# Kernel tuning notes

Hardware: AMD Instinct MI355X
Metric: run time of the kernel (lower is better)

The kernel has to match this reference:

```python
import jax, jax.numpy as jnp
import numpy as np

BATCH = 65536
NUM_OBS = 64
LATENT = 64
HID = (512, 512, 256)


def _mlp(x, W1, b1, W2, b2, W3, b3, W4, b4):
    # torch Linear: y = x @ W.T + b, ELU activations between hidden layers
    h = jax.nn.elu(x @ W1.T + b1)
    h = jax.nn.elu(h @ W2.T + b2)
    h = jax.nn.elu(h @ W3.T + b3)
    return h @ W4.T + b4  # [B, LATENT]


def setup_inputs() -> dict:
    key = jax.random.key(0)
    ks = jax.random.split(key, 9)
    def w(k, shape, fan_in):
        return jax.random.normal(k, shape, dtype=jnp.float32) * (1.0 / np.sqrt(fan_in))
    return {
        "x": jax.random.normal(ks[0], (BATCH, NUM_OBS), dtype=jnp.float32),
        "W1": w(ks[1], (HID[0], NUM_OBS), NUM_OBS),
        "b1": jnp.zeros((HID[0],), jnp.float32),
        "W2": w(ks[2], (HID[1], HID[0]), HID[0]),
        "b2": jnp.zeros((HID[1],), jnp.float32),
        "W3": w(ks[3], (HID[2], HID[1]), HID[1]),
        "b3": jnp.zeros((HID[2],), jnp.float32),
        "W4": w(ks[4], (LATENT, HID[2]), HID[2]),
        "b4": jnp.zeros((LATENT,), jnp.float32),
    }


def reference(x, W1, b1, W2, b2, W3, b3, W4, b4):
    sign = -1.0  # minimize=False -> sign = -1
    z = _mlp(x, W1, b1, W2, b2, W3, b3, W4, b4)          # [B, L]
    A = jnp.einsum('bi,bj->bij', z, z)                    # outer product [B, L, L]
    x_off = x - jnp.zeros_like(x)                         # offset_NN is zeros (no offset_hidden_dims)
    value = sign * jnp.einsum('bi,bij,bj->b', x_off, A, x_off)  # x^T A x, squeezed
    return value
```

## Files before the change

### kernel.cpp

```cpp
#include <hip/hip_runtime.h>


#define DEVI __device__ __forceinline__

typedef __attribute__((ext_vector_type(4))) float f32x4;
typedef __attribute__((ext_vector_type(8))) short bf16x8;

#define PADW 520
#define ROWS 64

DEVI short f2bf(float f) {
  unsigned u = __float_as_uint(f);
  u = u + 0x7fffu + ((u >> 16) & 1u);
  return (short)(u >> 16);
}

__global__ void cvtw_all_kernel(const float* __restrict__ W1, const float* __restrict__ W2,
                                const float* __restrict__ W3, const float* __restrict__ W4,
                                short* __restrict__ dst) {
  int i = blockIdx.x * blockDim.x + threadIdx.x;
  if (i >= 110592) return;
  const float* src;
  int off;
  if (i < 8192)        { src = W1; off = 0; }
  else if (i < 73728)  { src = W2; off = 8192; }
  else if (i < 106496) { src = W3; off = 73728; }
  else                 { src = W4; off = 106496; }
  float4 v = reinterpret_cast<const float4*>(src)[i - off];
  short4 o;
  o.x = f2bf(v.x); o.y = f2bf(v.y); o.z = f2bf(v.z); o.w = f2bf(v.w);
  reinterpret_cast<short4*>(dst)[i] = o;
}

template<int K, int NCT, bool DO_ELU>
DEVI void mlp_layer(const short* __restrict__ Wb, const float* __restrict__ bias,
                    short (&hb)[ROWS][PADW], int wn, int lane) {
  const int lr = lane & 15, kg = lane >> 4;
  const int c0 = wn * (NCT * 16);
  f32x4 acc[4][NCT] = {};
  for (int ks = 0; ks < K / 32; ++ks) {
    const int kk = ks * 32 + kg * 8;
    bf16x8 a[4], b[NCT];
#pragma unroll
    for (int rt = 0; rt < 4; ++rt)
      a[rt] = *reinterpret_cast<const bf16x8*>(&hb[rt * 16 + lr][kk]);
#pragma unroll
    for (int ct = 0; ct < NCT; ++ct)
      b[ct] = *reinterpret_cast<const bf16x8*>(&Wb[(c0 + ct * 16 + lr) * K + kk]);
#pragma unroll
    for (int rt = 0; rt < 4; ++rt)
#pragma unroll
      for (int ct = 0; ct < NCT; ++ct)
        acc[rt][ct] = __builtin_amdgcn_mfma_f32_16x16x32_bf16(a[rt], b[ct], acc[rt][ct], 0, 0, 0);
  }
  __syncthreads();
#pragma unroll
  for (int ct = 0; ct < NCT; ++ct) {
    const int col = c0 + ct * 16 + lr;
    const float bv = bias[col];
#pragma unroll
    for (int rt = 0; rt < 4; ++rt) {
#pragma unroll
      for (int j = 0; j < 4; ++j) {
        float v = acc[rt][ct][j] + bv;
        if (DO_ELU) v = v > 0.f ? v : (__expf(v) - 1.f);
        hb[rt * 16 + kg * 4 + j][col] = f2bf(v);
      }
    }
  }
  __syncthreads();
}

DEVI void final_layer(const short* __restrict__ W4b, const float* __restrict__ b4,
                      const float* __restrict__ xg, float* __restrict__ out,
                      short (&hb)[ROWS][PADW], int wid, int lane, int R0) {
  const int lr = lane & 15, kg = lane >> 4;
  const int r0 = wid * 16;
  f32x4 acc[4] = {};
  for (int ks = 0; ks < 8; ++ks) {
    const int kk = ks * 32 + kg * 8;
    bf16x8 a = *reinterpret_cast<const bf16x8*>(&hb[r0 + lr][kk]);
#pragma unroll
    for (int ct = 0; ct < 4; ++ct) {
      bf16x8 b = *reinterpret_cast<const bf16x8*>(&W4b[(ct * 16 + lr) * 256 + kk]);
      acc[ct] = __builtin_amdgcn_mfma_f32_16x16x32_bf16(a, b, acc[ct], 0, 0, 0);
    }
  }
  float bv[4];
#pragma unroll
  for (int ct = 0; ct < 4; ++ct) bv[ct] = b4[ct * 16 + lr];
#pragma unroll
  for (int j = 0; j < 4; ++j) {
    const int gr = R0 + r0 + kg * 4 + j;
    float p = 0.f;
#pragma unroll
    for (int ct = 0; ct < 4; ++ct)
      p += (acc[ct][j] + bv[ct]) * xg[gr * 64 + ct * 16 + lr];
    p += __shfl_xor(p, 1);
    p += __shfl_xor(p, 2);
    p += __shfl_xor(p, 4);
    p += __shfl_xor(p, 8);
    if (lr == 0) out[gr] = -p * p;
  }
}

__global__ __launch_bounds__(512, 4)
void mlp_fused_kernel(const float* __restrict__ x,
                      const short* __restrict__ Wb,
                      const float* __restrict__ b1, const float* __restrict__ b2,
                      const float* __restrict__ b3, const float* __restrict__ b4,
                      float* __restrict__ out) {
  __shared__ __align__(16) short hb[ROWS][PADW];
  const int tid = threadIdx.x;
  const int lane = tid & 63, wid = tid >> 6;
  const int R0 = blockIdx.x * ROWS;

#pragma unroll
  for (int s = 0; s < 2; ++s) {
    const int f = tid + s * 512;
    const int r = f >> 4, c4 = f & 15;
    float4 v = reinterpret_cast<const float4*>(x)[R0 * 16 + f];
    short4 o;
    o.x = f2bf(v.x); o.y = f2bf(v.y); o.z = f2bf(v.z); o.w = f2bf(v.w);
    *reinterpret_cast<short4*>(&hb[r][c4 * 4]) = o;
  }
  __syncthreads();

  const short* W1b = Wb;
  const short* W2b = Wb + 32768;
  const short* W3b = Wb + 32768 + 262144;
  const short* W4b = Wb + 32768 + 262144 + 131072;

  mlp_layer<64, 4, true>(W1b, b1, hb, wid, lane);
  mlp_layer<512, 4, true>(W2b, b2, hb, wid, lane);
  mlp_layer<512, 2, true>(W3b, b3, hb, wid, lane);
  if (wid < 4)
    final_layer(W4b, b4, x, out, hb, wid, lane, R0);
}

extern "C" void kernel_launch(void* const* d_in, const int* in_sizes, int n_in,
                              void* d_out, int out_size, void* d_ws, size_t ws_size,
                              hipStream_t stream) {
  const float* x  = (const float*)d_in[0];
  const float* W1 = (const float*)d_in[1];
  const float* b1 = (const float*)d_in[2];
  const float* W2 = (const float*)d_in[3];
  const float* b2 = (const float*)d_in[4];
  const float* W3 = (const float*)d_in[5];
  const float* b3 = (const float*)d_in[6];
  const float* W4 = (const float*)d_in[7];
  const float* b4 = (const float*)d_in[8];
  float* out = (float*)d_out;
  short* wsb = (short*)d_ws;

  cvtw_all_kernel<<<432, 256, 0, stream>>>(W1, W2, W3, W4, wsb);
  mlp_fused_kernel<<<1024, 512, 0, stream>>>(x, wsb, b1, b2, b3, b4, out);
}
```

Before: 194.8 us.

## Double-buffer weight k-slices in LDS via async global_load_lds prefetch

Weight tiles for each 32-wide k-step are now copied asynchronously into two swizzled LDS buffers with global_load_lds, and the next slice is prefetched while the current one feeds MFMA. Prefetching crosses layer boundaries, so the first slice of the next layer loads during the last step of the current one. The intent is to hide global and L2 latency on the weight operand and avoid bank conflicts through an XOR swizzle. The cost is an extra 64KB of LDS per block, which lowers occupancy (launch bounds drop from 4 to 2), and a block-wide barrier on every k-step. Each wave still consumes only its own columns, so the staging adds no data reuse.

```diff
diff --git a/kernel.cpp b/kernel.cpp
--- a/kernel.cpp
+++ b/kernel.cpp
@@ -32,13 +32,38 @@
   reinterpret_cast<short4*>(dst)[i] = o;
 }
 
-template<int K, int NCT, bool DO_ELU>
-DEVI void mlp_layer(const short* __restrict__ Wb, const float* __restrict__ bias,
-                    short (&hb)[ROWS][PADW], int wn, int lane) {
-  const int lr = lane & 15, kg = lane >> 4;
-  const int c0 = wn * (NCT * 16);
+DEVI void gld16(const void* g, void* l) {
+  __builtin_amdgcn_global_load_lds((const __attribute__((address_space(1))) void*)g,
+                                   (__attribute__((address_space(3))) void*)l, 16, 0, 0);
+}
+
+template<int COLS, int K>
+DEVI void stage_w(const short* __restrict__ W, int ks, short* dst, int tid) {
+#pragma unroll
+  for (int i = 0; i < COLS / 128; ++i) {
+    const int G = i * 512 + tid;
+    const int c = G >> 2, gp = G & 3;
+    const int g = gp ^ ((c >> 1) & 3);
+    gld16(W + c * K + ks * 32 + g * 8, dst + G * 8);
+  }
+}
+
+template<int K, int NCT, int NEXT_COLS, int NEXT_K>
+DEVI void hidden_layer(const short* __restrict__ W, const short* __restrict__ Wn,
+                       const float* __restrict__ bias,
+                       short (&hb)[ROWS][PADW], short* wta, short* wtb, int& cur,
+                       int tid, int wid, int lr, int kg) {
+  const int c0 = wid * (NCT * 16);
+  const int swz = (kg ^ ((lr >> 1) & 3)) * 16;
+  constexpr int NKS = K / 32;
   f32x4 acc[4][NCT] = {};
-  for (int ks = 0; ks < K / 32; ++ks) {
+  for (int ks = 0; ks < NKS; ++ks) {
+    short* nxt = cur ? wta : wtb;
+    const short* src = cur ? wtb : wta;
+    if (ks + 1 < NKS)
+      stage_w<NCT * 128, K>(W, ks + 1, nxt, tid);
+    else if constexpr (NEXT_COLS > 0)
+      stage_w<NEXT_COLS, NEXT_K>(Wn, 0, nxt, tid);
     const int kk = ks * 32 + kg * 8;
     bf16x8 a[4], b[NCT];
 #pragma unroll
@@ -46,14 +71,16 @@
       a[rt] = *reinterpret_cast<const bf16x8*>(&hb[rt * 16 + lr][kk]);
 #pragma unroll
     for (int ct = 0; ct < NCT; ++ct)
-      b[ct] = *reinterpret_cast<const bf16x8*>(&Wb[(c0 + ct * 16 + lr) * K + kk]);
+      b[ct] = *reinterpret_cast<const bf16x8*>(
+          (const char*)src + (c0 + ct * 16 + lr) * 64 + swz);
 #pragma unroll
     for (int rt = 0; rt < 4; ++rt)
 #pragma unroll
       for (int ct = 0; ct < NCT; ++ct)
         acc[rt][ct] = __builtin_amdgcn_mfma_f32_16x16x32_bf16(a[rt], b[ct], acc[rt][ct], 0, 0, 0);
+    __syncthreads();
+    cur ^= 1;
   }
-  __syncthreads();
 #pragma unroll
   for (int ct = 0; ct < NCT; ++ct) {
     const int col = c0 + ct * 16 + lr;
@@ -63,7 +90,7 @@
 #pragma unroll
       for (int j = 0; j < 4; ++j) {
         float v = acc[rt][ct][j] + bv;
-        if (DO_ELU) v = v > 0.f ? v : (__expf(v) - 1.f);
+        v = v > 0.f ? v : (__expf(v) - 1.f);
         hb[rt * 16 + kg * 4 + j][col] = f2bf(v);
       }
     }
@@ -104,16 +131,23 @@
   }
 }
 
-__global__ __launch_bounds__(512, 4)
+__global__ __launch_bounds__(512, 2)
 void mlp_fused_kernel(const float* __restrict__ x,
                       const short* __restrict__ Wb,
                       const float* __restrict__ b1, const float* __restrict__ b2,
                       const float* __restrict__ b3, const float* __restrict__ b4,
                       float* __restrict__ out) {
   __shared__ __align__(16) short hb[ROWS][PADW];
+  __shared__ __align__(16) short wt[2][512 * 32];
   const int tid = threadIdx.x;
   const int lane = tid & 63, wid = tid >> 6;
+  const int lr = lane & 15, kg = lane >> 4;
   const int R0 = blockIdx.x * ROWS;
+
+  const short* W1b = Wb;
+  const short* W2b = Wb + 32768;
+  const short* W3b = Wb + 32768 + 262144;
+  const short* W4b = Wb + 32768 + 262144 + 131072;
 
 #pragma unroll
   for (int s = 0; s < 2; ++s) {
@@ -124,16 +158,13 @@
     o.x = f2bf(v.x); o.y = f2bf(v.y); o.z = f2bf(v.z); o.w = f2bf(v.w);
     *reinterpret_cast<short4*>(&hb[r][c4 * 4]) = o;
   }
+  stage_w<512, 64>(W1b, 0, wt[0], tid);
   __syncthreads();
 
-  const short* W1b = Wb;
-  const short* W2b = Wb + 32768;
-  const short* W3b = Wb + 32768 + 262144;
-  const short* W4b = Wb + 32768 + 262144 + 131072;
-
-  mlp_layer<64, 4, true>(W1b, b1, hb, wid, lane);
-  mlp_layer<512, 4, true>(W2b, b2, hb, wid, lane);
-  mlp_layer<512, 2, true>(W3b, b3, hb, wid, lane);
+  int cur = 0;
+  hidden_layer<64, 4, 512, 512>(W1b, W2b, b1, hb, wt[0], wt[1], cur, tid, wid, lr, kg);
+  hidden_layer<512, 4, 256, 512>(W2b, W3b, b2, hb, wt[0], wt[1], cur, tid, wid, lr, kg);
+  hidden_layer<512, 2, 0, 0>(W3b, nullptr, b3, hb, wt[0], wt[1], cur, tid, wid, lr, kg);
   if (wid < 4)
     final_layer(W4b, b4, x, out, hb, wid, lane, R0);
 }
```

New measurement: 191.6 us. Within noise of the previous version (-1.7%).
